# Optimization experiments

Measured on AMD Instinct MI355X. Metric: run time of the kernel, lower is better.

Reference implementation:

```python
import jax, jax.numpy as jnp
import numpy as np

C_CURV = 1.0          # Poincare ball curvature
EPS = 1e-5
MAX_NORM = (1.0 - 1e-4) / np.sqrt(C_CURV)


def _artanh(x):
    x = jnp.clip(x, -1.0 + 1e-5, 1.0 - 1e-5)
    return 0.5 * (jnp.log1p(x) - jnp.log1p(-x))


def _expmap0(v):
    # v: [N,C,H,W]; norm over channel dim per spatial location
    n = jnp.maximum(jnp.linalg.norm(v, axis=1, keepdims=True), EPS)
    sc = np.sqrt(C_CURV)
    return jnp.tanh(sc * n) * v / (sc * n)


def _logmap0(y):
    n = jnp.maximum(jnp.linalg.norm(y, axis=1, keepdims=True), EPS)
    sc = np.sqrt(C_CURV)
    return _artanh(sc * n) * y / (sc * n)


def _project(y):
    # clamp back inside the ball
    n = jnp.maximum(jnp.linalg.norm(y, axis=1, keepdims=True), EPS)
    return jnp.where(n > MAX_NORM, y * (MAX_NORM / n), y)


def _conv3x3(u, w, b):
    y = jax.lax.conv_general_dilated(u, w, window_strides=(1, 1),
                                     padding=((1, 1), (1, 1)),
                                     dimension_numbers=('NCHW', 'OIHW', 'NCHW'))
    return y + b[None, :, None, None]


def _hconv(x, w, b):
    # HConvolution2d: tangent-space conv around origin
    return _project(_expmap0(_conv3x3(_logmap0(x), w, b)))


def _hbn(x, gamma, beta):
    # HBatchNorm2d: Euclidean BN in the tangent space at the origin (training stats)
    u = _logmap0(x)
    m = u.mean(axis=(0, 2, 3), keepdims=True)
    v = u.var(axis=(0, 2, 3), keepdims=True)
    u = (u - m) / jnp.sqrt(v + 1e-5)
    u = u * gamma[None, :, None, None] + beta[None, :, None, None]
    return _project(_expmap0(u))


def _hrelu(x):
    return _project(_expmap0(jax.nn.relu(_logmap0(x))))


def setup_inputs() -> dict:
    key = jax.random.key(0)
    ks = jax.random.split(key, 8)
    N, Cin, Cmid, Cout, H, W = 8, 32, 32, 32, 256, 256
    # input point on the Poincare ball
    x = _project(_expmap0(0.1 * jax.random.normal(ks[0], (N, Cin, H, W), jnp.float32)))
    fan1 = Cin * 9
    fan2 = Cmid * 9
    w1 = jax.random.normal(ks[1], (Cmid, Cin, 3, 3), jnp.float32) / np.sqrt(fan1)
    b1 = jnp.zeros((Cmid,), jnp.float32)
    g1 = jnp.ones((Cmid,), jnp.float32)
    beta1 = jnp.zeros((Cmid,), jnp.float32)
    w2 = jax.random.normal(ks[2], (Cout, Cmid, 3, 3), jnp.float32) / np.sqrt(fan2)
    b2 = jnp.zeros((Cout,), jnp.float32)
    g2 = jnp.ones((Cout,), jnp.float32)
    beta2 = jnp.zeros((Cout,), jnp.float32)
    return {"x": x, "w1": w1, "b1": b1, "g1": g1, "beta1": beta1,
            "w2": w2, "b2": b2, "g2": g2, "beta2": beta2}


def reference(x, w1, b1, g1, beta1, w2, b2, g2, beta2):
    out = _hconv(x, w1, b1)
    out = _hbn(out, g1, beta1)
    out = _hrelu(out)
    out = _hconv(out, w2, b2)
    out = _hbn(out, g2, beta2)
    out = _hrelu(out)
    return out
```

## Files before the change

kernel.cpp:

```cpp
#include <hip/hip_runtime.h>
#include <math.h>

#define HWDIM 256
#define CH 32
#define NB 8
#define TILE 16
#define NLOC (NB*HWDIM*HWDIM)
#define R_CLAMP 4.9517189f
#define MAXN 0.9999f
#define BN_EPS 1e-5f
#define EPSF 1e-5f
#define NBLK 2048
#define OST 264

typedef __attribute__((ext_vector_type(8))) _Float16 half8;
typedef __attribute__((ext_vector_type(4))) _Float16 half4;
typedef __attribute__((ext_vector_type(4))) float floatx4;

__device__ __forceinline__ float artanh_fast(float n) {
    float t = fminf(n, 1.0f - 1e-5f);
    return 0.5f * __logf(__fdividef(1.0f + t, 1.0f - t));
}

__global__ __launch_bounds__(256) void wprep_kernel(
    const float* __restrict__ w1, const float* __restrict__ w2,
    _Float16* __restrict__ wp1, _Float16* __restrict__ wp2)
{
    int idx = blockIdx.x * 256 + threadIdx.x;
    if (idx >= 2*CH*CH*9) return;
    int s = idx >= CH*CH*9;
    int id = idx - s*(CH*CH*9);
    const float* w = s ? w2 : w1;
    _Float16* wp = s ? wp2 : wp1;
    int j  = id & 7;
    int r  = id >> 3;
    int co = r & 31;
    int og = r >> 5;
    int g  = og & 3;
    int o  = og >> 2;
    int ci = g*8 + j;
    wp[id] = (_Float16)w[(co*CH + ci)*9 + o];
}

template<int STAGE>
__global__ __launch_bounds__(256) void conv_mfma_kernel(
    const void* __restrict__ srcv,
    const _Float16* __restrict__ wp,
    const float* __restrict__ bias,
    const float* __restrict__ scsh,
    _Float16* __restrict__ dst,
    float* __restrict__ partials)
{
    __shared__ _Float16 ah[10368];
    __shared__ float red[4][64];

    const int tid = threadIdx.x;
    const int flat = blockIdx.x;
    const int bz = flat & 7;
    const int t  = flat >> 3;
    const int by = t >> 4, bx = t & 15;
    const int h0 = by*TILE - 1, w0 = bx*TILE - 1;

    #pragma unroll 1
    for (int loc = tid; loc < 324; loc += 256) {
        int y = loc / 18, x = loc - y*18;
        int gh = h0 + y, gw = w0 + x;
        if (gh < 0 || gh >= HWDIM || gw < 0 || gw >= HWDIM) {
            half8 z = {0,0,0,0,0,0,0,0};
            #pragma unroll
            for (int g = 0; g < 4; g++) *(half8*)(ah + ((y*4+g)*18 + x)*8) = z;
            continue;
        }
        float v[CH]; float n2 = 0.f;
        if (STAGE == 1) {
            const float* p = (const float*)srcv + ((size_t)bz*CH << 16) + gh*HWDIM + gw;
            #pragma unroll
            for (int c = 0; c < CH; c++) { float t0 = p[(size_t)c << 16]; v[c] = t0; n2 = fmaf(t0, t0, n2); }
            float n = fmaxf(sqrtf(n2), EPSF);
            float f = __fdividef(artanh_fast(n), n);
            #pragma unroll
            for (int c = 0; c < CH; c++) v[c] *= f;
        } else {
            const _Float16* p = (const _Float16*)srcv + (((size_t)bz << 16) + gh*HWDIM + gw)*CH;
            half8 raw[4];
            #pragma unroll
            for (int k = 0; k < 4; k++) raw[k] = *(const half8*)(p + 8*k);
            #pragma unroll
            for (int c = 0; c < CH; c++) {
                float t0 = fmaf((float)raw[c>>3][c&7], scsh[c], scsh[CH + c]);
                v[c] = t0; n2 = fmaf(t0, t0, n2);
            }
            float n = sqrtf(n2);
            float f = (n > R_CLAMP) ? __fdividef(R_CLAMP, n) : 1.0f;
            #pragma unroll
            for (int c = 0; c < CH; c++) v[c] = fmaxf(v[c]*f, 0.0f);
        }
        #pragma unroll
        for (int g = 0; g < 4; g++) {
            half8 hv;
            #pragma unroll
            for (int j = 0; j < 8; j++) hv[j] = (_Float16)v[g*8 + j];
            *(half8*)(ah + ((y*4+g)*18 + x)*8) = hv;
        }
    }
    __syncthreads();

    const int lane = tid & 63, wave = tid >> 6;
    const int xx = lane & 15, q = lane >> 4;

    floatx4 acc[4][2];
    #pragma unroll
    for (int i = 0; i < 4; i++) {
        acc[i][0] = (floatx4){0.f,0.f,0.f,0.f};
        acc[i][1] = (floatx4){0.f,0.f,0.f,0.f};
    }

    __builtin_amdgcn_s_setprio(1);
    #pragma unroll
    for (int dx = 0; dx < 3; dx++) {
        half8 af[6];
        #pragma unroll
        for (int yy = 0; yy < 6; yy++)
            af[yy] = *(const half8*)(ah + (((wave*4+yy)*4 + q)*18 + xx + dx)*8);
        #pragma unroll
        for (int dy = 0; dy < 3; dy++) {
            const int o = dy*3 + dx;
            const _Float16* wb = wp + (size_t)((o*4 + q)*32)*8;
            half8 wf0 = *(const half8*)(wb + xx*8);
            half8 wf1 = *(const half8*)(wb + (xx+16)*8);
            #pragma unroll
            for (int i = 0; i < 4; i++) {
                acc[i][0] = __builtin_amdgcn_mfma_f32_16x16x32_f16(wf0, af[i+dy], acc[i][0], 0,0,0);
                acc[i][1] = __builtin_amdgcn_mfma_f32_16x16x32_f16(wf1, af[i+dy], acc[i][1], 0,0,0);
            }
        }
    }
    __builtin_amdgcn_s_setprio(0);

    float bs[8];
    #pragma unroll
    for (int r = 0; r < 4; r++) { bs[r] = bias[q*4+r]; bs[4+r] = bias[q*4+r+16]; }
    float sv[8], qv[8];
    #pragma unroll
    for (int k = 0; k < 8; k++) { sv[k] = 0.f; qv[k] = 0.f; }

    _Float16* dp = dst + (((size_t)bz << 16) + (size_t)(by*TILE)*HWDIM + bx*TILE + xx)*CH + q*4;

    #pragma unroll
    for (int i = 0; i < 4; i++) {
        float n2 = 0.f;
        #pragma unroll
        for (int r = 0; r < 4; r++) {
            acc[i][0][r] += bs[r];
            acc[i][1][r] += bs[4+r];
            n2 = fmaf(acc[i][0][r], acc[i][0][r], n2);
            n2 = fmaf(acc[i][1][r], acc[i][1][r], n2);
        }
        n2 += __shfl_xor(n2, 16, 64);
        n2 += __shfl_xor(n2, 32, 64);
        float nn = sqrtf(n2);
        float f = (nn > R_CLAMP) ? __fdividef(R_CLAMP, nn) : 1.0f;
        half4 o0, o1;
        #pragma unroll
        for (int r = 0; r < 4; r++) {
            float a0 = acc[i][0][r] * f;
            float a1 = acc[i][1][r] * f;
            sv[r]   += a0; qv[r]   = fmaf(a0, a0, qv[r]);
            sv[4+r] += a1; qv[4+r] = fmaf(a1, a1, qv[4+r]);
            o0[r] = (_Float16)a0; o1[r] = (_Float16)a1;
        }
        _Float16* a = dp + (size_t)(wave*4 + i)*HWDIM*CH;
        *(half4*)(a)      = o0;
        *(half4*)(a + 16) = o1;
    }

    #pragma unroll
    for (int k = 0; k < 8; k++) {
        #pragma unroll
        for (int m = 1; m < 16; m <<= 1) {
            sv[k] += __shfl_xor(sv[k], m, 64);
            qv[k] += __shfl_xor(qv[k], m, 64);
        }
    }
    if (xx == 0) {
        #pragma unroll
        for (int r = 0; r < 4; r++) {
            red[wave][q*4+r]        = sv[r];
            red[wave][16 + q*4+r]   = sv[4+r];
            red[wave][32 + q*4+r]   = qv[r];
            red[wave][48 + q*4+r]   = qv[4+r];
        }
    }
    __syncthreads();
    if (tid < 64) {
        float s = red[0][tid] + red[1][tid] + red[2][tid] + red[3][tid];
        partials[(size_t)tid*NBLK + flat] = s;
    }
}

__global__ __launch_bounds__(256) void finalize_kernel(
    const float* __restrict__ partials,
    const float* __restrict__ g, const float* __restrict__ beta,
    float* __restrict__ scsh)
{
    __shared__ float ss[256], sq[256];
    const int c = blockIdx.x;
    const int tid = threadIdx.x;
    float s = 0.f, q = 0.f;
    for (int b = tid; b < NBLK; b += 256) {
        s += partials[(size_t)c*NBLK + b];
        q += partials[(size_t)(CH + c)*NBLK + b];
    }
    ss[tid] = s; sq[tid] = q;
    __syncthreads();
    for (int st = 128; st > 0; st >>= 1) {
        if (tid < st) { ss[tid] += ss[tid+st]; sq[tid] += sq[tid+st]; }
        __syncthreads();
    }
    if (tid == 0) {
        const float NS = (float)NLOC;
        float mean = ss[0] / NS;
        float var = fmaxf(sq[0] / NS - mean*mean, 0.0f);
        float sc = g[c] / sqrtf(var + BN_EPS);
        scsh[c] = sc;
        scsh[CH + c] = beta[c] - mean*sc;
    }
}

__global__ __launch_bounds__(256) void out_kernel(
    const _Float16* __restrict__ t4c, const float* __restrict__ scsh,
    float* __restrict__ out)
{
    __shared__ float outb[16*OST];
    const int w = threadIdx.x;
    const int h = blockIdx.x, n = blockIdx.y;
    const _Float16* p = t4c + (((size_t)n << 16) + (size_t)h*HWDIM + w)*CH;
    half8 raw[4];
    #pragma unroll
    for (int k = 0; k < 4; k++) raw[k] = *(const half8*)(p + 8*k);
    float u[CH]; float n2 = 0.f;
    #pragma unroll
    for (int c = 0; c < CH; c++) {
        float t = fmaf((float)raw[c>>3][c&7], scsh[c], scsh[CH+c]);
        u[c] = t; n2 = fmaf(t, t, n2);
    }
    float nn = sqrtf(n2);
    float f = (nn > R_CLAMP) ? __fdividef(R_CLAMP, nn) : 1.0f;
    float r2 = 0.f;
    #pragma unroll
    for (int c = 0; c < CH; c++) { float r = fmaxf(u[c]*f, 0.0f); u[c] = r; r2 = fmaf(r, r, r2); }
    float rn = fmaxf(sqrtf(r2), EPSF);
    float a = __expf(2.0f * rn);
    float th = __fdividef(a - 1.0f, a + 1.0f);
    float s = __fdividef(fminf(th, MAXN), rn);
    #pragma unroll
    for (int c = 0; c < CH; c++) u[c] *= s;

    #pragma unroll
    for (int hf = 0; hf < 2; hf++) {
        if (hf) __syncthreads();
        #pragma unroll
        for (int c = 0; c < 16; c++) outb[c*OST + w] = u[hf*16 + c];
        __syncthreads();
        int co = threadIdx.x >> 4, seg = threadIdx.x & 15;
        const float* row = outb + co*OST + seg*16;
        float* gp = out + ((size_t)(n*CH + hf*16 + co) << 16) + (size_t)h*HWDIM + seg*16;
        #pragma unroll
        for (int k = 0; k < 4; k++) *(floatx4*)(gp + 4*k) = *(const floatx4*)(row + 4*k);
    }
}

extern "C" void kernel_launch(void* const* d_in, const int* in_sizes, int n_in,
                              void* d_out, int out_size, void* d_ws, size_t ws_size,
                              hipStream_t stream)
{
    const float* x   = (const float*)d_in[0];
    const float* w1  = (const float*)d_in[1];
    const float* b1  = (const float*)d_in[2];
    const float* g1  = (const float*)d_in[3];
    const float* be1 = (const float*)d_in[4];
    const float* w2  = (const float*)d_in[5];
    const float* b2  = (const float*)d_in[6];
    const float* g2  = (const float*)d_in[7];
    const float* be2 = (const float*)d_in[8];
    float* outf = (float*)d_out;

    char* ws = (char*)d_ws;
    _Float16* wp1   = (_Float16*)ws;
    _Float16* wp2   = wp1 + 9216;
    float* partials = (float*)(ws + 36864);
    float* scsh1    = (float*)(ws + 36864 + 524288);
    float* scsh2    = scsh1 + 64;
    _Float16* t1c   = (_Float16*)(scsh2 + 64);
    _Float16* t4c   = t1c + (size_t)NLOC*CH;

    wprep_kernel<<<72, 256, 0, stream>>>(w1, w2, wp1, wp2);

    conv_mfma_kernel<1><<<NBLK, 256, 0, stream>>>(x, wp1, b1, scsh1, t1c, partials);
    finalize_kernel<<<32, 256, 0, stream>>>(partials, g1, be1, scsh1);
    conv_mfma_kernel<2><<<NBLK, 256, 0, stream>>>(t1c, wp2, b2, scsh1, t4c, partials);
    finalize_kernel<<<32, 256, 0, stream>>>(partials, g2, be2, scsh2);
    out_kernel<<<dim3(HWDIM, NB), 256, 0, stream>>>(t4c, scsh2, outf);
}
```

Measured before the change: 200.8 us.

## Replace BN finalize kernels with atomic stat accumulation and in-kernel scale computation

Each conv block now atomically adds its per-channel sum and sum-of-squares partials into a small global stats buffer instead of writing per-block partials. The consumer kernels derive the BN scale and shift from these totals into shared memory, so the two finalize kernel launches go away. The stats buffer is zeroed inside the weight-prep kernel. In exchange there are 64 atomics per block on 64 shared addresses, which may contend, and the float summation order is no longer deterministic.

```diff
diff --git a/kernel.cpp b/kernel.cpp
--- a/kernel.cpp
+++ b/kernel.cpp
@@ -24,9 +24,11 @@
 
 __global__ __launch_bounds__(256) void wprep_kernel(
     const float* __restrict__ w1, const float* __restrict__ w2,
-    _Float16* __restrict__ wp1, _Float16* __restrict__ wp2)
+    _Float16* __restrict__ wp1, _Float16* __restrict__ wp2,
+    float* __restrict__ gstat)
 {
     int idx = blockIdx.x * 256 + threadIdx.x;
+    if (blockIdx.x == 0 && threadIdx.x < 128) gstat[threadIdx.x] = 0.f;
     if (idx >= 2*CH*CH*9) return;
     int s = idx >= CH*CH*9;
     int id = idx - s*(CH*CH*9);
@@ -47,12 +49,14 @@
     const void* __restrict__ srcv,
     const _Float16* __restrict__ wp,
     const float* __restrict__ bias,
-    const float* __restrict__ scsh,
+    const float* __restrict__ gstat_in,
+    const float* __restrict__ gamma, const float* __restrict__ beta,
     _Float16* __restrict__ dst,
-    float* __restrict__ partials)
+    float* __restrict__ gstat_out)
 {
     __shared__ _Float16 ah[10368];
     __shared__ float red[4][64];
+    __shared__ float scshL[64];
 
     const int tid = threadIdx.x;
     const int flat = blockIdx.x;
@@ -61,6 +65,20 @@
     const int by = t >> 4, bx = t & 15;
     const int h0 = by*TILE - 1, w0 = bx*TILE - 1;
 
+    if (STAGE == 2) {
+        if (tid < 32) {
+            float sum = gstat_in[tid];
+            float sq  = gstat_in[32 + tid];
+            const float NS = (float)NLOC;
+            float mean = sum / NS;
+            float var = fmaxf(sq / NS - mean*mean, 0.0f);
+            float sc = gamma[tid] * __frsqrt_rn(var + BN_EPS);
+            scshL[tid] = sc;
+            scshL[32 + tid] = beta[tid] - mean*sc;
+        }
+        __syncthreads();
+    }
+
     #pragma unroll 1
     for (int loc = tid; loc < 324; loc += 256) {
         int y = loc / 18, x = loc - y*18;
@@ -87,7 +105,7 @@
             for (int k = 0; k < 4; k++) raw[k] = *(const half8*)(p + 8*k);
             #pragma unroll
             for (int c = 0; c < CH; c++) {
-                float t0 = fmaf((float)raw[c>>3][c&7], scsh[c], scsh[CH + c]);
+                float t0 = fmaf((float)raw[c>>3][c&7], scshL[c], scshL[CH + c]);
                 v[c] = t0; n2 = fmaf(t0, t0, n2);
             }
             float n = sqrtf(n2);
@@ -194,46 +212,33 @@
     __syncthreads();
     if (tid < 64) {
         float s = red[0][tid] + red[1][tid] + red[2][tid] + red[3][tid];
-        partials[(size_t)tid*NBLK + flat] = s;
-    }
-}
-
-__global__ __launch_bounds__(256) void finalize_kernel(
-    const float* __restrict__ partials,
-    const float* __restrict__ g, const float* __restrict__ beta,
-    float* __restrict__ scsh)
-{
-    __shared__ float ss[256], sq[256];
-    const int c = blockIdx.x;
-    const int tid = threadIdx.x;
-    float s = 0.f, q = 0.f;
-    for (int b = tid; b < NBLK; b += 256) {
-        s += partials[(size_t)c*NBLK + b];
-        q += partials[(size_t)(CH + c)*NBLK + b];
-    }
-    ss[tid] = s; sq[tid] = q;
-    __syncthreads();
-    for (int st = 128; st > 0; st >>= 1) {
-        if (tid < st) { ss[tid] += ss[tid+st]; sq[tid] += sq[tid+st]; }
-        __syncthreads();
-    }
-    if (tid == 0) {
-        const float NS = (float)NLOC;
-        float mean = ss[0] / NS;
-        float var = fmaxf(sq[0] / NS - mean*mean, 0.0f);
-        float sc = g[c] / sqrtf(var + BN_EPS);
-        scsh[c] = sc;
-        scsh[CH + c] = beta[c] - mean*sc;
+        atomicAdd(&gstat_out[tid], s);
     }
 }
 
 __global__ __launch_bounds__(256) void out_kernel(
-    const _Float16* __restrict__ t4c, const float* __restrict__ scsh,
+    const _Float16* __restrict__ t4c,
+    const float* __restrict__ gstat,
+    const float* __restrict__ gamma, const float* __restrict__ beta,
     float* __restrict__ out)
 {
     __shared__ float outb[16*OST];
+    __shared__ float scshL[64];
     const int w = threadIdx.x;
     const int h = blockIdx.x, n = blockIdx.y;
+
+    if (w < 32) {
+        float sum = gstat[w];
+        float sq  = gstat[32 + w];
+        const float NS = (float)NLOC;
+        float mean = sum / NS;
+        float var = fmaxf(sq / NS - mean*mean, 0.0f);
+        float sc = gamma[w] * __frsqrt_rn(var + BN_EPS);
+        scshL[w] = sc;
+        scshL[32 + w] = beta[w] - mean*sc;
+    }
+    __syncthreads();
+
     const _Float16* p = t4c + (((size_t)n << 16) + (size_t)h*HWDIM + w)*CH;
     half8 raw[4];
     #pragma unroll
@@ -241,7 +246,7 @@
     float u[CH]; float n2 = 0.f;
     #pragma unroll
     for (int c = 0; c < CH; c++) {
-        float t = fmaf((float)raw[c>>3][c&7], scsh[c], scsh[CH+c]);
+        float t = fmaf((float)raw[c>>3][c&7], scshL[c], scshL[CH+c]);
         u[c] = t; n2 = fmaf(t, t, n2);
     }
     float nn = sqrtf(n2);
@@ -258,7 +263,7 @@
 
     #pragma unroll
     for (int hf = 0; hf < 2; hf++) {
-        if (hf) __syncthreads();
+        __syncthreads();
         #pragma unroll
         for (int c = 0; c < 16; c++) outb[c*OST + w] = u[hf*16 + c];
         __syncthreads();
@@ -288,17 +293,14 @@
     char* ws = (char*)d_ws;
     _Float16* wp1   = (_Float16*)ws;
     _Float16* wp2   = wp1 + 9216;
-    float* partials = (float*)(ws + 36864);
-    float* scsh1    = (float*)(ws + 36864 + 524288);
-    float* scsh2    = scsh1 + 64;
-    _Float16* t1c   = (_Float16*)(scsh2 + 64);
+    float* gstatA   = (float*)(ws + 36864);
+    float* gstatB   = gstatA + 64;
+    _Float16* t1c   = (_Float16*)(ws + 37632);
     _Float16* t4c   = t1c + (size_t)NLOC*CH;
 
-    wprep_kernel<<<72, 256, 0, stream>>>(w1, w2, wp1, wp2);
-
-    conv_mfma_kernel<1><<<NBLK, 256, 0, stream>>>(x, wp1, b1, scsh1, t1c, partials);
-    finalize_kernel<<<32, 256, 0, stream>>>(partials, g1, be1, scsh1);
-    conv_mfma_kernel<2><<<NBLK, 256, 0, stream>>>(t1c, wp2, b2, scsh1, t4c, partials);
-    finalize_kernel<<<32, 256, 0, stream>>>(partials, g2, be2, scsh2);
-    out_kernel<<<dim3(HWDIM, NB), 256, 0, stream>>>(t4c, scsh2, outf);
-}
+    wprep_kernel<<<72, 256, 0, stream>>>(w1, w2, wp1, wp2, gstatA);
+
+    conv_mfma_kernel<1><<<NBLK, 256, 0, stream>>>(x,   wp1, b1, nullptr, nullptr, nullptr, t1c, gstatA);
+    conv_mfma_kernel<2><<<NBLK, 256, 0, stream>>>(t1c, wp2, b2, gstatA, g1, be1,          t4c, gstatB);
+    out_kernel<<<dim3(HWDIM, NB), 256, 0, stream>>>(t4c, gstatB, g2, be2, outf);
+}
```

Result: slower. 256.6 us (+27.8%).

## Double-buffer second conv with async global-to-LDS loads over four tiles per block

Applied to the files above, without the earlier changes.

Splits the templated conv into a stage-1 kernel and a new stage-2 kernel. In the new kernel each block handles four horizontal tiles, keeps the conv weights resident in LDS, and prefetches the next tile's halo with global_load_lds while computing the current one. The BN-apply/relu transform is then done in place in LDS. This aims to hide global memory latency and cut weight reloads, at the cost of much more LDS per block (lower occupancy) and a quarter as many blocks. Halo rows are clamped and the raw reads are overwritten with zeros at borders.

```diff
diff --git a/kernel.cpp b/kernel.cpp
--- a/kernel.cpp
+++ b/kernel.cpp
@@ -11,6 +11,7 @@
 #define BN_EPS 1e-5f
 #define EPSF 1e-5f
 #define NBLK 2048
+#define NBLK2 512
 #define OST 264
 
 typedef __attribute__((ext_vector_type(8))) _Float16 half8;
@@ -42,12 +43,10 @@
     wp[id] = (_Float16)w[(co*CH + ci)*9 + o];
 }
 
-template<int STAGE>
-__global__ __launch_bounds__(256) void conv_mfma_kernel(
-    const void* __restrict__ srcv,
+__global__ __launch_bounds__(256) void conv1_kernel(
+    const float* __restrict__ src,
     const _Float16* __restrict__ wp,
     const float* __restrict__ bias,
-    const float* __restrict__ scsh,
     _Float16* __restrict__ dst,
     float* __restrict__ partials)
 {
@@ -72,34 +71,16 @@
             continue;
         }
         float v[CH]; float n2 = 0.f;
-        if (STAGE == 1) {
-            const float* p = (const float*)srcv + ((size_t)bz*CH << 16) + gh*HWDIM + gw;
-            #pragma unroll
-            for (int c = 0; c < CH; c++) { float t0 = p[(size_t)c << 16]; v[c] = t0; n2 = fmaf(t0, t0, n2); }
-            float n = fmaxf(sqrtf(n2), EPSF);
-            float f = __fdividef(artanh_fast(n), n);
-            #pragma unroll
-            for (int c = 0; c < CH; c++) v[c] *= f;
-        } else {
-            const _Float16* p = (const _Float16*)srcv + (((size_t)bz << 16) + gh*HWDIM + gw)*CH;
-            half8 raw[4];
-            #pragma unroll
-            for (int k = 0; k < 4; k++) raw[k] = *(const half8*)(p + 8*k);
-            #pragma unroll
-            for (int c = 0; c < CH; c++) {
-                float t0 = fmaf((float)raw[c>>3][c&7], scsh[c], scsh[CH + c]);
-                v[c] = t0; n2 = fmaf(t0, t0, n2);
-            }
-            float n = sqrtf(n2);
-            float f = (n > R_CLAMP) ? __fdividef(R_CLAMP, n) : 1.0f;
-            #pragma unroll
-            for (int c = 0; c < CH; c++) v[c] = fmaxf(v[c]*f, 0.0f);
-        }
+        const float* p = src + ((size_t)bz*CH << 16) + gh*HWDIM + gw;
+        #pragma unroll
+        for (int c = 0; c < CH; c++) { float t0 = p[(size_t)c << 16]; v[c] = t0; n2 = fmaf(t0, t0, n2); }
+        float n = fmaxf(sqrtf(n2), EPSF);
+        float f = __fdividef(artanh_fast(n), n);
         #pragma unroll
         for (int g = 0; g < 4; g++) {
             half8 hv;
             #pragma unroll
-            for (int j = 0; j < 8; j++) hv[j] = (_Float16)v[g*8 + j];
+            for (int j = 0; j < 8; j++) hv[j] = (_Float16)(v[g*8 + j] * f);
             *(half8*)(ah + ((y*4+g)*18 + x)*8) = hv;
         }
     }
@@ -198,8 +179,203 @@
     }
 }
 
+__global__ __launch_bounds__(256) void conv2_dma_kernel(
+    const _Float16* __restrict__ src,
+    const _Float16* __restrict__ wp,
+    const float* __restrict__ bias,
+    const float* __restrict__ scsh,
+    _Float16* __restrict__ dst,
+    float* __restrict__ partials)
+{
+    __shared__ _Float16 wlds[9216];
+    __shared__ _Float16 A[2][10368];
+    __shared__ float red[4][64];
+
+    const int tid = threadIdx.x;
+    const int b   = blockIdx.x;
+    const int bz  = b & 7;
+    const int tb  = b >> 3;
+    const int by  = tb >> 2;
+    const int bx0 = (tb & 3) * 4;
+    const int h0  = by*TILE - 1;
+
+    const int lane = tid & 63, wave = tid >> 6;
+    const int xx = lane & 15, q = lane >> 4;
+
+    for (int i = tid; i < 1152; i += 256)
+        *(half8*)(wlds + (size_t)i*8) = *(const half8*)(wp + (size_t)i*8);
+
+    #define STAGE_ISSUE(jj, bb) do {                                                       \
+        const int w0_ = (bx0 + (jj))*TILE - 1;                                             \
+        half8 lreg_ = {0,0,0,0,0,0,0,0};                                                   \
+        if (tid < 16) {                                                                    \
+            int gh_ = h0 + 17, gw_ = w0_ + 2 + tid;                                        \
+            int ghc_ = gh_ < 0 ? 0 : (gh_ > 255 ? 255 : gh_);                              \
+            int gwc_ = gw_ < 0 ? 0 : (gw_ > 255 ? 255 : gw_);                              \
+            lreg_ = *(const half8*)(src + (((size_t)bz << 16) + ghc_*HWDIM + gwc_)*CH + 24); \
+        }                                                                                  \
+        _Pragma("unroll")                                                                  \
+        for (int k_ = 0; k_ < 5; k_++) {                                                   \
+            int it_ = (k_*4 + wave)*64 + lane;                                             \
+            int y_ = it_ / 72; int rm_ = it_ - y_*72;                                      \
+            int g_ = rm_ / 18; int x_ = rm_ - g_*18;                                       \
+            int gh_ = h0 + y_, gw_ = w0_ + x_;                                             \
+            int ghc_ = gh_ < 0 ? 0 : (gh_ > 255 ? 255 : gh_);                              \
+            int gwc_ = gw_ < 0 ? 0 : (gw_ > 255 ? 255 : gw_);                              \
+            const _Float16* gp_ = src + (((size_t)bz << 16) + ghc_*HWDIM + gwc_)*CH + g_*8; \
+            __builtin_amdgcn_global_load_lds(                                              \
+                (const __attribute__((address_space(1))) void*)gp_,                        \
+                (__attribute__((address_space(3))) void*)(&A[bb][0] + (size_t)((k_*4 + wave)*64)*8), \
+                16, 0, 0);                                                                 \
+        }                                                                                  \
+        if (tid < 16) *(half8*)(&A[bb][(size_t)(1280 + tid)*8]) = lreg_;                   \
+    } while (0)
+
+    float bs[8];
+    #pragma unroll
+    for (int r = 0; r < 4; r++) { bs[r] = bias[q*4+r]; bs[4+r] = bias[q*4+r+16]; }
+    float sv[8], qv[8];
+    #pragma unroll
+    for (int k = 0; k < 8; k++) { sv[k] = 0.f; qv[k] = 0.f; }
+
+    STAGE_ISSUE(0, 0);
+
+    #pragma unroll 1
+    for (int j = 0; j < 4; j++) {
+        const int cur = j & 1;
+        if (j + 1 < 4) {
+            STAGE_ISSUE(j + 1, cur ^ 1);
+            asm volatile("s_waitcnt vmcnt(5)" ::: "memory");
+        } else {
+            asm volatile("s_waitcnt vmcnt(0)" ::: "memory");
+        }
+        asm volatile("s_waitcnt lgkmcnt(0)" ::: "memory");
+        __builtin_amdgcn_s_barrier();
+        __builtin_amdgcn_sched_barrier(0);
+
+        const int w0 = (bx0 + j)*TILE - 1;
+        #pragma unroll 1
+        for (int loc = tid; loc < 324; loc += 256) {
+            int y = loc / 18, x = loc - y*18;
+            int gh = h0 + y, gw = w0 + x;
+            _Float16* b0 = &A[cur][(size_t)((y*4)*18 + x)*8];
+            if (gh < 0 || gh >= HWDIM || gw < 0 || gw >= HWDIM) {
+                half8 z = {0,0,0,0,0,0,0,0};
+                #pragma unroll
+                for (int g = 0; g < 4; g++) *(half8*)(b0 + g*144) = z;
+                continue;
+            }
+            half8 raw[4];
+            #pragma unroll
+            for (int g = 0; g < 4; g++) raw[g] = *(const half8*)(b0 + g*144);
+            float v[CH]; float n2 = 0.f;
+            #pragma unroll
+            for (int c = 0; c < CH; c++) {
+                float t0 = fmaf((float)raw[c>>3][c&7], scsh[c], scsh[CH + c]);
+                v[c] = t0; n2 = fmaf(t0, t0, n2);
+            }
+            float n = sqrtf(n2);
+            float f = (n > R_CLAMP) ? __fdividef(R_CLAMP, n) : 1.0f;
+            #pragma unroll
+            for (int g = 0; g < 4; g++) {
+                half8 hv;
+                #pragma unroll
+                for (int jj = 0; jj < 8; jj++) hv[jj] = (_Float16)fmaxf(v[g*8 + jj]*f, 0.0f);
+                *(half8*)(b0 + g*144) = hv;
+            }
+        }
+        asm volatile("s_waitcnt lgkmcnt(0)" ::: "memory");
+        __builtin_amdgcn_s_barrier();
+        __builtin_amdgcn_sched_barrier(0);
+
+        floatx4 acc[4][2];
+        #pragma unroll
+        for (int i = 0; i < 4; i++) {
+            acc[i][0] = (floatx4){0.f,0.f,0.f,0.f};
+            acc[i][1] = (floatx4){0.f,0.f,0.f,0.f};
+        }
+        __builtin_amdgcn_s_setprio(1);
+        #pragma unroll
+        for (int dx = 0; dx < 3; dx++) {
+            half8 af[6];
+            #pragma unroll
+            for (int yy = 0; yy < 6; yy++)
+                af[yy] = *(const half8*)(&A[cur][(size_t)(((wave*4+yy)*4 + q)*18 + xx + dx)*8]);
+            #pragma unroll
+            for (int dy = 0; dy < 3; dy++) {
+                const int o = dy*3 + dx;
+                const _Float16* wb = wlds + (size_t)((o*4 + q)*32)*8;
+                half8 wf0 = *(const half8*)(wb + xx*8);
+                half8 wf1 = *(const half8*)(wb + (xx+16)*8);
+                #pragma unroll
+                for (int i = 0; i < 4; i++) {
+                    acc[i][0] = __builtin_amdgcn_mfma_f32_16x16x32_f16(wf0, af[i+dy], acc[i][0], 0,0,0);
+                    acc[i][1] = __builtin_amdgcn_mfma_f32_16x16x32_f16(wf1, af[i+dy], acc[i][1], 0,0,0);
+                }
+            }
+        }
+        __builtin_amdgcn_s_setprio(0);
+
+        _Float16* dp = dst + (((size_t)bz << 16) + (size_t)(by*TILE)*HWDIM + (bx0 + j)*TILE + xx)*CH + q*4;
+        #pragma unroll
+        for (int i = 0; i < 4; i++) {
+            float n2 = 0.f;
+            #pragma unroll
+            for (int r = 0; r < 4; r++) {
+                acc[i][0][r] += bs[r];
+                acc[i][1][r] += bs[4+r];
+                n2 = fmaf(acc[i][0][r], acc[i][0][r], n2);
+                n2 = fmaf(acc[i][1][r], acc[i][1][r], n2);
+            }
+            n2 += __shfl_xor(n2, 16, 64);
+            n2 += __shfl_xor(n2, 32, 64);
+            float nn = sqrtf(n2);
+            float f = (nn > R_CLAMP) ? __fdividef(R_CLAMP, nn) : 1.0f;
+            half4 o0, o1;
+            #pragma unroll
+            for (int r = 0; r < 4; r++) {
+                float a0 = acc[i][0][r] * f;
+                float a1 = acc[i][1][r] * f;
+                sv[r]   += a0; qv[r]   = fmaf(a0, a0, qv[r]);
+                sv[4+r] += a1; qv[4+r] = fmaf(a1, a1, qv[4+r]);
+                o0[r] = (_Float16)a0; o1[r] = (_Float16)a1;
+            }
+            _Float16* a = dp + (size_t)(wave*4 + i)*HWDIM*CH;
+            *(half4*)(a)      = o0;
+            *(half4*)(a + 16) = o1;
+        }
+        asm volatile("s_waitcnt lgkmcnt(0)" ::: "memory");
+        __builtin_amdgcn_s_barrier();
+        __builtin_amdgcn_sched_barrier(0);
+    }
+    #undef STAGE_ISSUE
+
+    #pragma unroll
+    for (int k = 0; k < 8; k++) {
+        #pragma unroll
+        for (int m = 1; m < 16; m <<= 1) {
+            sv[k] += __shfl_xor(sv[k], m, 64);
+            qv[k] += __shfl_xor(qv[k], m, 64);
+        }
+    }
+    if (xx == 0) {
+        #pragma unroll
+        for (int r = 0; r < 4; r++) {
+            red[wave][q*4+r]        = sv[r];
+            red[wave][16 + q*4+r]   = sv[4+r];
+            red[wave][32 + q*4+r]   = qv[r];
+            red[wave][48 + q*4+r]   = qv[4+r];
+        }
+    }
+    __syncthreads();
+    if (tid < 64) {
+        float s = red[0][tid] + red[1][tid] + red[2][tid] + red[3][tid];
+        partials[(size_t)tid*NBLK + b] = s;
+    }
+}
+
 __global__ __launch_bounds__(256) void finalize_kernel(
-    const float* __restrict__ partials,
+    const float* __restrict__ partials, int nblk,
     const float* __restrict__ g, const float* __restrict__ beta,
     float* __restrict__ scsh)
 {
@@ -207,7 +383,7 @@
     const int c = blockIdx.x;
     const int tid = threadIdx.x;
     float s = 0.f, q = 0.f;
-    for (int b = tid; b < NBLK; b += 256) {
+    for (int b = tid; b < nblk; b += 256) {
         s += partials[(size_t)c*NBLK + b];
         q += partials[(size_t)(CH + c)*NBLK + b];
     }
@@ -296,9 +472,9 @@
 
     wprep_kernel<<<72, 256, 0, stream>>>(w1, w2, wp1, wp2);
 
-    conv_mfma_kernel<1><<<NBLK, 256, 0, stream>>>(x, wp1, b1, scsh1, t1c, partials);
-    finalize_kernel<<<32, 256, 0, stream>>>(partials, g1, be1, scsh1);
-    conv_mfma_kernel<2><<<NBLK, 256, 0, stream>>>(t1c, wp2, b2, scsh1, t4c, partials);
-    finalize_kernel<<<32, 256, 0, stream>>>(partials, g2, be2, scsh2);
+    conv1_kernel<<<NBLK, 256, 0, stream>>>(x, wp1, b1, t1c, partials);
+    finalize_kernel<<<32, 256, 0, stream>>>(partials, NBLK, g1, be1, scsh1);
+    conv2_dma_kernel<<<NBLK2, 256, 0, stream>>>(t1c, wp2, b2, scsh1, t4c, partials);
+    finalize_kernel<<<32, 256, 0, stream>>>(partials, NBLK2, g2, be2, scsh2);
     out_kernel<<<dim3(HWDIM, NB), 256, 0, stream>>>(t4c, scsh2, outf);
 }
```

Measured after the change: 201.5 us. Within noise of the previous version (+0.4%).
